# Kernel tuning notes

Hardware: AMD Instinct MI355X
Metric: run time of the kernel (lower is better)

The kernel has to match this reference:

```python
import jax, jax.numpy as jnp
import numpy as np

N, E = 50000, 800000
IN_C, HID, HEADS, LAT = 128, 64, 2, 32
NEG_SLOPE = 0.2  # PyG GATConv default LeakyReLU slope


def gat_layer(x, src, dst, W, att_src, att_dst, bias, heads, out_ch, concat, n):
    # Linear projection, per-head: [n, heads, out_ch]
    h = (x @ W).reshape(n, heads, out_ch)
    a_src = jnp.einsum('nhc,hc->nh', h, att_src)  # [n, heads]
    a_dst = jnp.einsum('nhc,hc->nh', h, att_dst)
    # Per-edge attention logits (edge j->i uses src j, dst i)
    alpha = jax.nn.leaky_relu(a_src[src] + a_dst[dst], negative_slope=NEG_SLOPE)  # [e, heads]
    # Segment softmax over incoming edges of each destination node
    amax = jax.ops.segment_max(alpha, dst, num_segments=n)
    ealpha = jnp.exp(alpha - amax[dst])
    denom = jax.ops.segment_sum(ealpha, dst, num_segments=n)
    alpha = ealpha / (denom[dst] + 1e-16)
    # Weighted scatter-aggregate of source features
    msg = h[src] * alpha[:, :, None]  # [e, heads, out_ch]
    out = jax.ops.segment_sum(msg, dst, num_segments=n)  # [n, heads, out_ch]
    out = out.reshape(n, heads * out_ch) if concat else out.mean(axis=1)
    return out + bias


def setup_inputs() -> dict:
    key = jax.random.key(0)
    ks = jax.random.split(key, 16)
    x = jax.random.normal(ks[0], (N, IN_C), dtype=jnp.float32)
    edge_index = jax.random.randint(ks[1], (2, E), 0, N, dtype=jnp.int32).astype(jnp.int64)
    s = 0.1
    W1 = jax.random.normal(ks[2], (IN_C, HEADS * HID), dtype=jnp.float32) * s
    att_src1 = jax.random.normal(ks[3], (HEADS, HID), dtype=jnp.float32) * s
    att_dst1 = jax.random.normal(ks[4], (HEADS, HID), dtype=jnp.float32) * s
    b1 = jnp.zeros((HEADS * HID,), dtype=jnp.float32)
    Wmu = jax.random.normal(ks[5], (HEADS * HID, LAT), dtype=jnp.float32) * s
    att_src_mu = jax.random.normal(ks[6], (1, LAT), dtype=jnp.float32) * s
    att_dst_mu = jax.random.normal(ks[7], (1, LAT), dtype=jnp.float32) * s
    bmu = jnp.zeros((LAT,), dtype=jnp.float32)
    Wlv = jax.random.normal(ks[8], (HEADS * HID, LAT), dtype=jnp.float32) * s
    att_src_lv = jax.random.normal(ks[9], (1, LAT), dtype=jnp.float32) * s
    att_dst_lv = jax.random.normal(ks[10], (1, LAT), dtype=jnp.float32) * s
    blv = jnp.zeros((LAT,), dtype=jnp.float32)
    return {"x": x, "edge_index": edge_index, "W1": W1, "att_src1": att_src1,
            "att_dst1": att_dst1, "b1": b1, "Wmu": Wmu, "att_src_mu": att_src_mu,
            "att_dst_mu": att_dst_mu, "bmu": bmu, "Wlv": Wlv,
            "att_src_lv": att_src_lv, "att_dst_lv": att_dst_lv, "blv": blv}


def reference(x, edge_index, W1, att_src1, att_dst1, b1,
              Wmu, att_src_mu, att_dst_mu, bmu,
              Wlv, att_src_lv, att_dst_lv, blv):
    n = x.shape[0]
    # PyG GATConv adds self-loops by default
    loops = jnp.arange(n, dtype=edge_index.dtype)
    src = jnp.concatenate([edge_index[0], loops])
    dst = jnp.concatenate([edge_index[1], loops])
    h = gat_layer(x, src, dst, W1, att_src1, att_dst1, b1, HEADS, HID, True, n)
    h = jax.nn.elu(h)
    mu = gat_layer(h, src, dst, Wmu, att_src_mu, att_dst_mu, bmu, 1, LAT, False, n)
    logvar = gat_layer(h, src, dst, Wlv, att_src_lv, att_dst_lv, blv, 1, LAT, False, n)
    return (mu, logvar)
```

## Files before the change

### kernel.cpp

```cpp
#include <hip/hip_runtime.h>
#include <hip/hip_bf16.h>

#define N_NODES 50000
#define N_EDGES 800000
#define EP (N_EDGES + N_NODES)
#define IN_C 128
#define HID 64
#define HEADS 2
#define LAT 32
#define NEG_SLOPE 0.2f
#define MAXDEG 256
#define NBUCKET 391
#define BCAP 3072
#define CHUNK 4096

typedef __attribute__((ext_vector_type(8))) short bf16x8;
typedef __attribute__((ext_vector_type(4))) float f32x4;

__device__ __forceinline__ unsigned short f2bf(float f) {
  unsigned u = __float_as_uint(f);
  u += 0x7FFF + ((u >> 16) & 1);
  return (unsigned short)(u >> 16);
}
__device__ __forceinline__ float bf_lo(unsigned u) { return __uint_as_float(u << 16); }
__device__ __forceinline__ float bf_hi(unsigned u) { return __uint_as_float(u & 0xFFFF0000u); }

__device__ __forceinline__ bf16x8 pack_bf8(const float* __restrict__ p) {
  float4 a = *(const float4*)p;
  float4 b = *(const float4*)(p + 4);
  bf16x8 r;
  r[0] = (short)f2bf(a.x); r[1] = (short)f2bf(a.y);
  r[2] = (short)f2bf(a.z); r[3] = (short)f2bf(a.w);
  r[4] = (short)f2bf(b.x); r[5] = (short)f2bf(b.y);
  r[6] = (short)f2bf(b.z); r[7] = (short)f2bf(b.w);
  return r;
}

__global__ void cursor_init_kernel(int* __restrict__ cursor) {
  int b = threadIdx.x;
  if (b < NBUCKET) cursor[b] = b * BCAP;
}

__global__ __launch_bounds__(256) void bucket_scatter_kernel(
    const int* __restrict__ ei, int* __restrict__ cursor,
    unsigned* __restrict__ csr) {
  __shared__ int histL[512];
  __shared__ int baseL[512];
  __shared__ int gbaseL[512];
  __shared__ int wsumS[4];
  __shared__ int nvalS;
  __shared__ unsigned staging[CHUNK];
  __shared__ unsigned short bktidL[CHUNK];
  const int t = threadIdx.x, lane = t & 63, wid = t >> 6;
  for (int i = t; i < 512; i += 256) histL[i] = 0;
  __syncthreads();
  int myb[CHUNK / 256];
  int myloc[CHUNK / 256];
  unsigned mypay[CHUNK / 256];
  #pragma unroll
  for (int i = 0; i < CHUNK / 256; ++i) {
    int e = blockIdx.x * CHUNK + i * 256 + t;
    if (e < EP) {
      int s, d;
      if (e < N_EDGES) { s = ei[e]; d = ei[N_EDGES + e]; }
      else { s = d = e - N_EDGES; }
      int b = d >> 7;
      myb[i] = b;
      mypay[i] = ((unsigned)(d & 127) << 17) | (unsigned)s;
      myloc[i] = atomicAdd(&histL[b], 1);
    } else myb[i] = -1;
  }
  __syncthreads();
  {
    int v0 = histL[2 * t], v1 = histL[2 * t + 1];
    int pair = v0 + v1, inc = pair;
    #pragma unroll
    for (int off = 1; off < 64; off <<= 1) {
      int nv = __shfl_up(inc, off);
      if (lane >= off) inc += nv;
    }
    if (lane == 63) wsumS[wid] = inc;
    __syncthreads();
    if (t == 0) {
      int run = 0;
      #pragma unroll
      for (int w = 0; w < 4; ++w) { int c = wsumS[w]; wsumS[w] = run; run += c; }
      nvalS = run;
    }
    __syncthreads();
    int excl = wsumS[wid] + inc - pair;
    baseL[2 * t] = excl;
    baseL[2 * t + 1] = excl + v0;
  }
  __syncthreads();
  #pragma unroll
  for (int i = 0; i < CHUNK / 256; ++i)
    if (myb[i] >= 0) {
      int p = baseL[myb[i]] + myloc[i];
      staging[p] = mypay[i];
      bktidL[p] = (unsigned short)myb[i];
    }
  for (int b = t; b < NBUCKET; b += 256) {
    int c = histL[b];
    gbaseL[b] = c ? atomicAdd(&cursor[b], c) : 0;
  }
  __syncthreads();
  const int nval = nvalS;
  for (int j = t; j < nval; j += 256) {
    int b = bktidL[j];
    int pos = gbaseL[b] + (j - baseL[b]);
    if (pos < (b + 1) * BCAP) csr[pos] = staging[j];
  }
}

__global__ __launch_bounds__(256) void bucket_fill_kernel(
    const int* __restrict__ cursor, unsigned* __restrict__ csr,
    int* __restrict__ counts, int* __restrict__ cend) {
  __shared__ unsigned eseg[BCAP];
  __shared__ int hist[128];
  __shared__ int basef[128];
  __shared__ int cur[128];
  const int b = blockIdx.x, t = threadIdx.x;
  const int segbase = b * BCAP;
  int cnt = cursor[b] - segbase;
  if (cnt > BCAP) cnt = BCAP;
  if (t < 128) hist[t] = 0;
  __syncthreads();
  for (int j = t; j < cnt; j += 256) {
    unsigned u = csr[segbase + j];
    eseg[j] = u;
    atomicAdd(&hist[u >> 17], 1);
  }
  __syncthreads();
  if (t < 64) {
    int v0 = hist[2 * t], v1 = hist[2 * t + 1];
    int pair = v0 + v1, inc = pair;
    #pragma unroll
    for (int off = 1; off < 64; off <<= 1) {
      int nv = __shfl_up(inc, off);
      if (t >= off) inc += nv;
    }
    int excl = inc - pair;
    basef[2 * t] = excl;
    basef[2 * t + 1] = excl + v0;
  }
  __syncthreads();
  if (t < 128) {
    cur[t] = basef[t];
    int n = b * 128 + t;
    if (n < N_NODES) {
      counts[n] = hist[t];
      cend[n] = segbase + basef[t] + hist[t];
    }
  }
  __syncthreads();
  for (int j = t; j < cnt; j += 256) {
    unsigned u = eseg[j];
    int dl = u >> 17;
    int p = atomicAdd(&cur[dl], 1);
    csr[segbase + p] = u & 0x1FFFF;
  }
}

__global__ __launch_bounds__(256) void proj1_kernel(
    const float* __restrict__ x, const float* __restrict__ W,
    unsigned short* __restrict__ h1b) {
  __shared__ unsigned short Wb[16384];
  const int t = threadIdx.x;
  for (int i = t; i < 128 * 128; i += 256) {
    int k = i >> 7, n = i & 127;
    int kk = k >> 5, q = (k >> 3) & 3, j = k & 7;
    Wb[((((kk << 2) + q) << 7) + n) * 8 + j] = f2bf(W[i]);
  }
  __syncthreads();
  const int w = t >> 6, lane = t & 63;
  const int m = lane & 15, quad = lane >> 4;
  const int row0 = blockIdx.x * 32;
  const int n0 = w * 32;
  f32x4 acc[2][2] = {};
  #pragma unroll
  for (int kk = 0; kk < 4; ++kk) {
    bf16x8 afr[2], bfr[2];
    #pragma unroll
    for (int mt = 0; mt < 2; ++mt) {
      int row = row0 + mt * 16 + m;
      if (row >= N_NODES) row = N_NODES - 1;
      afr[mt] = pack_bf8(x + (size_t)row * 128 + kk * 32 + quad * 8);
    }
    #pragma unroll
    for (int nt = 0; nt < 2; ++nt)
      bfr[nt] = *(const bf16x8*)&Wb[((((kk << 2) + quad) << 7) + n0 + nt * 16 + m) * 8];
    #pragma unroll
    for (int mt = 0; mt < 2; ++mt)
      #pragma unroll
      for (int nt = 0; nt < 2; ++nt)
        acc[mt][nt] = __builtin_amdgcn_mfma_f32_16x16x32_bf16(
            afr[mt], bfr[nt], acc[mt][nt], 0, 0, 0);
  }
  #pragma unroll
  for (int mt = 0; mt < 2; ++mt)
    #pragma unroll
    for (int r = 0; r < 4; ++r) {
      int row = row0 + mt * 16 + quad * 4 + r;
      if (row < N_NODES) {
        #pragma unroll
        for (int nt = 0; nt < 2; ++nt)
          h1b[(size_t)row * 128 + n0 + nt * 16 + m] = f2bf(acc[mt][nt][r]);
      }
    }
}

__global__ __launch_bounds__(256) void a1_kernel(
    const unsigned* __restrict__ h1b2, const float* __restrict__ att_src,
    const float* __restrict__ att_dst, float* __restrict__ a1) {
  const int n = blockIdx.x * 4 + (threadIdx.x >> 6);
  const int lane = threadIdx.x & 63;
  unsigned u = h1b2[(size_t)n * 64 + lane];
  float h0 = bf_lo(u), h1v = bf_hi(u);
  int head = lane >> 5;
  int cc = (lane * 2) & 63;
  float s = h0 * att_src[head * HID + cc] + h1v * att_src[head * HID + cc + 1];
  float d = h0 * att_dst[head * HID + cc] + h1v * att_dst[head * HID + cc + 1];
  #pragma unroll
  for (int off = 16; off; off >>= 1) {
    s += __shfl_xor(s, off);
    d += __shfl_xor(d, off);
  }
  if ((lane & 31) == 0) {
    a1[n * 4 + head] = s;
    a1[n * 4 + 2 + head] = d;
  }
}

__global__ __launch_bounds__(64) void agg1_csr_kernel(
    const int* __restrict__ counts, const int* __restrict__ cend,
    const unsigned* __restrict__ csr_src, const float4* __restrict__ a1,
    const unsigned* __restrict__ h1b2, const float* __restrict__ b,
    float* __restrict__ hact) {
  __shared__ float w_lds[2][MAXDEG];
  __shared__ int   s_lds[MAXDEG];
  const int n = blockIdx.x;
  const int t = threadIdx.x;
  const int end = cend[n];
  int cnt = counts[n];
  if (cnt > MAXDEG) cnt = MAXDEG;
  const int beg = end - cnt;
  const float4 bv = a1[n];
  float p0 = 0.f, p1 = 0.f;
  for (int i = t; i < cnt; i += 64) {
    int s = (int)csr_src[beg + i];
    float4 av = a1[s];
    float l0 = av.x + bv.z; l0 = l0 > 0.f ? l0 : NEG_SLOPE * l0;
    float l1 = av.y + bv.w; l1 = l1 > 0.f ? l1 : NEG_SLOPE * l1;
    float e0 = expf(l0), e1 = expf(l1);
    w_lds[0][i] = e0; w_lds[1][i] = e1; s_lds[i] = s;
    p0 += e0; p1 += e1;
  }
  #pragma unroll
  for (int off = 32; off; off >>= 1) {
    p0 += __shfl_xor(p0, off);
    p1 += __shfl_xor(p1, off);
  }
  __syncthreads();
  const int head = t >> 5;
  const unsigned* hp = h1b2 + t;
  float ax = 0.f, ay = 0.f;
  #pragma unroll 4
  for (int i = 0; i < cnt; ++i) {
    int s = s_lds[i];
    float w = w_lds[head][i];
    unsigned u = hp[(size_t)s * 64];
    ax += bf_lo(u) * w; ay += bf_hi(u) * w;
  }
  float inv = 1.f / ((head ? p1 : p0) + 1e-16f);
  float vx = ax * inv + b[t * 2];
  float vy = ay * inv + b[t * 2 + 1];
  vx = vx > 0.f ? vx : (expf(vx) - 1.f);
  vy = vy > 0.f ? vy : (expf(vy) - 1.f);
  *(float2*)(hact + (size_t)n * 128 + t * 2) = make_float2(vx, vy);
}

__global__ __launch_bounds__(256) void proj2_kernel(
    const float* __restrict__ h, const float* __restrict__ Wmu,
    const float* __restrict__ Wlv, unsigned short* __restrict__ h2b) {
  __shared__ unsigned short Wb[8192];
  const int t = threadIdx.x;
  for (int i = t; i < 128 * 64; i += 256) {
    int k = i >> 6, n = i & 63;
    float v = (n < 32) ? Wmu[k * 32 + n] : Wlv[k * 32 + (n - 32)];
    int kk = k >> 5, q = (k >> 3) & 3, j = k & 7;
    Wb[((((kk << 2) + q) << 6) + n) * 8 + j] = f2bf(v);
  }
  __syncthreads();
  const int w = t >> 6, lane = t & 63;
  const int m = lane & 15, quad = lane >> 4;
  const int row0 = blockIdx.x * 64 + (w >> 1) * 32;
  const int n0 = (w & 1) * 32;
  f32x4 acc[2][2] = {};
  #pragma unroll
  for (int kk = 0; kk < 4; ++kk) {
    bf16x8 afr[2], bfr[2];
    #pragma unroll
    for (int mt = 0; mt < 2; ++mt) {
      int row = row0 + mt * 16 + m;
      if (row >= N_NODES) row = N_NODES - 1;
      afr[mt] = pack_bf8(h + (size_t)row * 128 + kk * 32 + quad * 8);
    }
    #pragma unroll
    for (int nt = 0; nt < 2; ++nt)
      bfr[nt] = *(const bf16x8*)&Wb[((((kk << 2) + quad) << 6) + n0 + nt * 16 + m) * 8];
    #pragma unroll
    for (int mt = 0; mt < 2; ++mt)
      #pragma unroll
      for (int nt = 0; nt < 2; ++nt)
        acc[mt][nt] = __builtin_amdgcn_mfma_f32_16x16x32_bf16(
            afr[mt], bfr[nt], acc[mt][nt], 0, 0, 0);
  }
  #pragma unroll
  for (int mt = 0; mt < 2; ++mt)
    #pragma unroll
    for (int r = 0; r < 4; ++r) {
      int row = row0 + mt * 16 + quad * 4 + r;
      if (row < N_NODES) {
        #pragma unroll
        for (int nt = 0; nt < 2; ++nt)
          h2b[(size_t)row * 64 + n0 + nt * 16 + m] = f2bf(acc[mt][nt][r]);
      }
    }
}

__global__ __launch_bounds__(256) void a2_kernel(
    const unsigned short* __restrict__ h2b, const float* __restrict__ asmu,
    const float* __restrict__ admu, const float* __restrict__ aslv,
    const float* __restrict__ adlv, float* __restrict__ a2) {
  const int n = blockIdx.x * 4 + (threadIdx.x >> 6);
  const int lane = threadIdx.x & 63;
  float h = __uint_as_float(((unsigned)h2b[(size_t)n * 64 + lane]) << 16);
  int j = lane >> 5, o = lane & 31;
  float s = h * (j ? aslv : asmu)[o];
  float d = h * (j ? adlv : admu)[o];
  #pragma unroll
  for (int off = 16; off; off >>= 1) {
    s += __shfl_xor(s, off);
    d += __shfl_xor(d, off);
  }
  if (o == 0) {
    a2[n * 4 + j * 2 + 0] = s;
    a2[n * 4 + j * 2 + 1] = d;
  }
}

__global__ __launch_bounds__(64) void agg2_csr_kernel(
    const int* __restrict__ counts, const int* __restrict__ cend,
    const unsigned* __restrict__ csr_src, const float4* __restrict__ a2,
    const unsigned short* __restrict__ h2b,
    const float* __restrict__ bmu, const float* __restrict__ blv,
    float* __restrict__ out) {
  __shared__ float w_lds[2][MAXDEG];
  __shared__ int   s_lds[MAXDEG];
  const int n = blockIdx.x;
  const int t = threadIdx.x;
  const int end = cend[n];
  int cnt = counts[n];
  if (cnt > MAXDEG) cnt = MAXDEG;
  const int beg = end - cnt;
  const float4 bv = a2[n];
  float p0 = 0.f, p1 = 0.f;
  for (int i = t; i < cnt; i += 64) {
    int s = (int)csr_src[beg + i];
    float4 av = a2[s];
    float l0 = av.x + bv.y; l0 = l0 > 0.f ? l0 : NEG_SLOPE * l0;
    float l1 = av.z + bv.w; l1 = l1 > 0.f ? l1 : NEG_SLOPE * l1;
    float e0 = expf(l0), e1 = expf(l1);
    w_lds[0][i] = e0; w_lds[1][i] = e1; s_lds[i] = s;
    p0 += e0; p1 += e1;
  }
  #pragma unroll
  for (int off = 32; off; off >>= 1) {
    p0 += __shfl_xor(p0, off);
    p1 += __shfl_xor(p1, off);
  }
  __syncthreads();
  const int j = t >> 5, o = t & 31;
  const unsigned short* hp = h2b + t;
  float acc = 0.f;
  #pragma unroll 4
  for (int i = 0; i < cnt; ++i) {
    int s = s_lds[i];
    float hv = __uint_as_float(((unsigned)hp[(size_t)s * 64]) << 16);
    acc += hv * w_lds[j][i];
  }
  float inv = 1.f / ((j ? p1 : p0) + 1e-16f);
  out[(size_t)j * N_NODES * LAT + (size_t)n * LAT + o] =
      acc * inv + (j ? blv : bmu)[o];
}

extern "C" void kernel_launch(void* const* d_in, const int* in_sizes, int n_in,
                              void* d_out, int out_size, void* d_ws, size_t ws_size,
                              hipStream_t stream) {
  const float* x        = (const float*)d_in[0];
  const int* ei         = (const int*)d_in[1];
  const float* W1       = (const float*)d_in[2];
  const float* att_src1 = (const float*)d_in[3];
  const float* att_dst1 = (const float*)d_in[4];
  const float* b1       = (const float*)d_in[5];
  const float* Wmu      = (const float*)d_in[6];
  const float* asmu     = (const float*)d_in[7];
  const float* admu     = (const float*)d_in[8];
  const float* bmu      = (const float*)d_in[9];
  const float* Wlv      = (const float*)d_in[10];
  const float* aslv     = (const float*)d_in[11];
  const float* adlv     = (const float*)d_in[12];
  const float* blv      = (const float*)d_in[13];
  float* out = (float*)d_out;

  float* ws   = (float*)d_ws;
  float* hact = ws;
  float* a1   = hact + (size_t)N_NODES * 128;
  float* a2   = a1 + (size_t)N_NODES * 4;
  unsigned short* h1b = (unsigned short*)(a2 + (size_t)N_NODES * 4);
  unsigned short* h2b = h1b + (size_t)N_NODES * 128;
  int* counts = (int*)(h2b + (size_t)N_NODES * 64);
  int* cend   = counts + N_NODES;
  int* cursor = cend + N_NODES;
  unsigned* csr = (unsigned*)(cursor + NBUCKET);

  cursor_init_kernel<<<1, 512, 0, stream>>>(cursor);
  bucket_scatter_kernel<<<(EP + CHUNK - 1) / CHUNK, 256, 0, stream>>>(ei, cursor, csr);
  bucket_fill_kernel<<<NBUCKET, 256, 0, stream>>>(cursor, csr, counts, cend);

  proj1_kernel<<<(N_NODES + 31) / 32, 256, 0, stream>>>(x, W1, h1b);
  a1_kernel<<<N_NODES / 4, 256, 0, stream>>>(
      (const unsigned*)h1b, att_src1, att_dst1, a1);
  agg1_csr_kernel<<<N_NODES, 64, 0, stream>>>(
      counts, cend, csr, (const float4*)a1, (const unsigned*)h1b, b1, hact);

  proj2_kernel<<<(N_NODES + 63) / 64, 256, 0, stream>>>(hact, Wmu, Wlv, h2b);
  a2_kernel<<<N_NODES / 4, 256, 0, stream>>>(h2b, asmu, admu, aslv, adlv, a2);
  agg2_csr_kernel<<<N_NODES, 64, 0, stream>>>(
      counts, cend, csr, (const float4*)a2, h2b, bmu, blv, out);
}
```

Before: 238.2 us.

## Fuse edge bucketing with layer-1 projection and fold attention logits into projections

Merges the edge bucket-scatter and layer-1 projection into one launch that splits blocks by index, sharing LDS through a union. The attention dot products (a1, a2) are now computed from the MFMA accumulators inside the projection kernels, so the separate a1/a2 kernels that re-read h1b/h2b are removed. Cursor init becomes a memset with relative offsets. This cuts four launches and two passes over the projected features, at the cost of LDS atomics and fp32-vs-bf16 logits that differ slightly from before.

After: 220.2 us. 1.08x faster.

```diff
diff --git a/kernel.cpp b/kernel.cpp
--- a/kernel.cpp
+++ b/kernel.cpp
@@ -13,6 +13,8 @@
 #define NBUCKET 391
 #define BCAP 3072
 #define CHUNK 4096
+#define NSCAT ((EP + CHUNK - 1) / CHUNK)
+#define NPROJ1 ((N_NODES + 31) / 32)
 
 typedef __attribute__((ext_vector_type(8))) short bf16x8;
 typedef __attribute__((ext_vector_type(4))) float f32x4;
@@ -36,80 +38,160 @@
   return r;
 }
 
-__global__ void cursor_init_kernel(int* __restrict__ cursor) {
-  int b = threadIdx.x;
-  if (b < NBUCKET) cursor[b] = b * BCAP;
-}
-
-__global__ __launch_bounds__(256) void bucket_scatter_kernel(
+struct ScatSmem {
+  int histL[512];
+  int baseL[512];
+  int gbaseL[512];
+  int wsumS[4];
+  int nvalS;
+  unsigned staging[CHUNK];
+  unsigned short bktidL[CHUNK];
+};
+struct Proj1Smem {
+  unsigned short Wb[16384];
+  float part[32][4];
+};
+union K1Smem { ScatSmem sc; Proj1Smem pj; };
+
+__global__ __launch_bounds__(256) void k1_kernel(
     const int* __restrict__ ei, int* __restrict__ cursor,
-    unsigned* __restrict__ csr) {
-  __shared__ int histL[512];
-  __shared__ int baseL[512];
-  __shared__ int gbaseL[512];
-  __shared__ int wsumS[4];
-  __shared__ int nvalS;
-  __shared__ unsigned staging[CHUNK];
-  __shared__ unsigned short bktidL[CHUNK];
+    unsigned* __restrict__ csr,
+    const float* __restrict__ x, const float* __restrict__ W,
+    const float* __restrict__ att_src, const float* __restrict__ att_dst,
+    unsigned short* __restrict__ h1b, float* __restrict__ a1) {
+  __shared__ K1Smem sm;
   const int t = threadIdx.x, lane = t & 63, wid = t >> 6;
-  for (int i = t; i < 512; i += 256) histL[i] = 0;
-  __syncthreads();
-  int myb[CHUNK / 256];
-  int myloc[CHUNK / 256];
-  unsigned mypay[CHUNK / 256];
-  #pragma unroll
-  for (int i = 0; i < CHUNK / 256; ++i) {
-    int e = blockIdx.x * CHUNK + i * 256 + t;
-    if (e < EP) {
-      int s, d;
-      if (e < N_EDGES) { s = ei[e]; d = ei[N_EDGES + e]; }
-      else { s = d = e - N_EDGES; }
-      int b = d >> 7;
-      myb[i] = b;
-      mypay[i] = ((unsigned)(d & 127) << 17) | (unsigned)s;
-      myloc[i] = atomicAdd(&histL[b], 1);
-    } else myb[i] = -1;
-  }
-  __syncthreads();
-  {
-    int v0 = histL[2 * t], v1 = histL[2 * t + 1];
-    int pair = v0 + v1, inc = pair;
-    #pragma unroll
-    for (int off = 1; off < 64; off <<= 1) {
-      int nv = __shfl_up(inc, off);
-      if (lane >= off) inc += nv;
-    }
-    if (lane == 63) wsumS[wid] = inc;
-    __syncthreads();
-    if (t == 0) {
-      int run = 0;
-      #pragma unroll
-      for (int w = 0; w < 4; ++w) { int c = wsumS[w]; wsumS[w] = run; run += c; }
-      nvalS = run;
-    }
-    __syncthreads();
-    int excl = wsumS[wid] + inc - pair;
-    baseL[2 * t] = excl;
-    baseL[2 * t + 1] = excl + v0;
-  }
-  __syncthreads();
-  #pragma unroll
-  for (int i = 0; i < CHUNK / 256; ++i)
-    if (myb[i] >= 0) {
-      int p = baseL[myb[i]] + myloc[i];
-      staging[p] = mypay[i];
-      bktidL[p] = (unsigned short)myb[i];
-    }
-  for (int b = t; b < NBUCKET; b += 256) {
-    int c = histL[b];
-    gbaseL[b] = c ? atomicAdd(&cursor[b], c) : 0;
-  }
-  __syncthreads();
-  const int nval = nvalS;
-  for (int j = t; j < nval; j += 256) {
-    int b = bktidL[j];
-    int pos = gbaseL[b] + (j - baseL[b]);
-    if (pos < (b + 1) * BCAP) csr[pos] = staging[j];
+
+  if (blockIdx.x < NSCAT) {
+    for (int i = t; i < 512; i += 256) sm.sc.histL[i] = 0;
+    __syncthreads();
+    int myb[CHUNK / 256];
+    int myloc[CHUNK / 256];
+    unsigned mypay[CHUNK / 256];
+    #pragma unroll
+    for (int i = 0; i < CHUNK / 256; ++i) {
+      int e = blockIdx.x * CHUNK + i * 256 + t;
+      if (e < EP) {
+        int s, d;
+        if (e < N_EDGES) { s = ei[e]; d = ei[N_EDGES + e]; }
+        else { s = d = e - N_EDGES; }
+        int b = d >> 7;
+        myb[i] = b;
+        mypay[i] = ((unsigned)(d & 127) << 17) | (unsigned)s;
+        myloc[i] = atomicAdd(&sm.sc.histL[b], 1);
+      } else myb[i] = -1;
+    }
+    __syncthreads();
+    {
+      int v0 = sm.sc.histL[2 * t], v1 = sm.sc.histL[2 * t + 1];
+      int pair = v0 + v1, inc = pair;
+      #pragma unroll
+      for (int off = 1; off < 64; off <<= 1) {
+        int nv = __shfl_up(inc, off);
+        if (lane >= off) inc += nv;
+      }
+      if (lane == 63) sm.sc.wsumS[wid] = inc;
+      __syncthreads();
+      if (t == 0) {
+        int run = 0;
+        #pragma unroll
+        for (int w = 0; w < 4; ++w) { int c = sm.sc.wsumS[w]; sm.sc.wsumS[w] = run; run += c; }
+        sm.sc.nvalS = run;
+      }
+      __syncthreads();
+      int excl = sm.sc.wsumS[wid] + inc - pair;
+      sm.sc.baseL[2 * t] = excl;
+      sm.sc.baseL[2 * t + 1] = excl + v0;
+    }
+    __syncthreads();
+    #pragma unroll
+    for (int i = 0; i < CHUNK / 256; ++i)
+      if (myb[i] >= 0) {
+        int p = sm.sc.baseL[myb[i]] + myloc[i];
+        sm.sc.staging[p] = mypay[i];
+        sm.sc.bktidL[p] = (unsigned short)myb[i];
+      }
+    for (int b = t; b < NBUCKET; b += 256) {
+      int c = sm.sc.histL[b];
+      sm.sc.gbaseL[b] = c ? atomicAdd(&cursor[b], c) : 0;
+    }
+    __syncthreads();
+    const int nval = sm.sc.nvalS;
+    for (int j = t; j < nval; j += 256) {
+      int b = sm.sc.bktidL[j];
+      int off = sm.sc.gbaseL[b] + (j - sm.sc.baseL[b]);
+      if (off < BCAP) csr[b * BCAP + off] = sm.sc.staging[j];
+    }
+  } else {
+    const int pb = blockIdx.x - NSCAT;
+    for (int i = t; i < 128 * 128; i += 256) {
+      int k = i >> 7, n = i & 127;
+      int kk = k >> 5, q = (k >> 3) & 3, j = k & 7;
+      sm.pj.Wb[((((kk << 2) + q) << 7) + n) * 8 + j] = f2bf(W[i]);
+    }
+    if (t < 128) ((float*)sm.pj.part)[t] = 0.f;
+    __syncthreads();
+    const int w = wid;
+    const int m = lane & 15, quad = lane >> 4;
+    const int row0 = pb * 32;
+    const int n0 = w * 32;
+    const int head = w >> 1;
+    f32x4 acc[2][2] = {};
+    #pragma unroll
+    for (int kk = 0; kk < 4; ++kk) {
+      bf16x8 afr[2], bfr[2];
+      #pragma unroll
+      for (int mt = 0; mt < 2; ++mt) {
+        int row = row0 + mt * 16 + m;
+        if (row >= N_NODES) row = N_NODES - 1;
+        afr[mt] = pack_bf8(x + (size_t)row * 128 + kk * 32 + quad * 8);
+      }
+      #pragma unroll
+      for (int nt = 0; nt < 2; ++nt)
+        bfr[nt] = *(const bf16x8*)&sm.pj.Wb[((((kk << 2) + quad) << 7) + n0 + nt * 16 + m) * 8];
+      #pragma unroll
+      for (int mt = 0; mt < 2; ++mt)
+        #pragma unroll
+        for (int nt = 0; nt < 2; ++nt)
+          acc[mt][nt] = __builtin_amdgcn_mfma_f32_16x16x32_bf16(
+              afr[mt], bfr[nt], acc[mt][nt], 0, 0, 0);
+    }
+    float asv[2], adv[2];
+    #pragma unroll
+    for (int nt = 0; nt < 2; ++nt) {
+      int cc = ((n0 & 63) + nt * 16 + m);
+      asv[nt] = att_src[head * HID + cc];
+      adv[nt] = att_dst[head * HID + cc];
+    }
+    #pragma unroll
+    for (int mt = 0; mt < 2; ++mt)
+      #pragma unroll
+      for (int r = 0; r < 4; ++r) {
+        int row = row0 + mt * 16 + quad * 4 + r;
+        if (row < N_NODES) {
+          #pragma unroll
+          for (int nt = 0; nt < 2; ++nt)
+            h1b[(size_t)row * 128 + n0 + nt * 16 + m] = f2bf(acc[mt][nt][r]);
+        }
+        float s = acc[mt][0][r] * asv[0] + acc[mt][1][r] * asv[1];
+        float d = acc[mt][0][r] * adv[0] + acc[mt][1][r] * adv[1];
+        #pragma unroll
+        for (int off = 8; off; off >>= 1) {
+          s += __shfl_xor(s, off);
+          d += __shfl_xor(d, off);
+        }
+        if (m == 0) {
+          atomicAdd(&sm.pj.part[mt * 16 + quad * 4 + r][head], s);
+          atomicAdd(&sm.pj.part[mt * 16 + quad * 4 + r][2 + head], d);
+        }
+      }
+    __syncthreads();
+    if (t < 32) {
+      int row = row0 + t;
+      if (row < N_NODES)
+        *(float4*)&a1[(size_t)row * 4] = make_float4(
+            sm.pj.part[t][0], sm.pj.part[t][1], sm.pj.part[t][2], sm.pj.part[t][3]);
+    }
   }
 }
 
@@ -122,7 +204,7 @@
   __shared__ int cur[128];
   const int b = blockIdx.x, t = threadIdx.x;
   const int segbase = b * BCAP;
-  int cnt = cursor[b] - segbase;
+  int cnt = cursor[b];
   if (cnt > BCAP) cnt = BCAP;
   if (t < 128) hist[t] = 0;
   __syncthreads();
@@ -159,76 +241,6 @@
     int dl = u >> 17;
     int p = atomicAdd(&cur[dl], 1);
     csr[segbase + p] = u & 0x1FFFF;
-  }
-}
-
-__global__ __launch_bounds__(256) void proj1_kernel(
-    const float* __restrict__ x, const float* __restrict__ W,
-    unsigned short* __restrict__ h1b) {
-  __shared__ unsigned short Wb[16384];
-  const int t = threadIdx.x;
-  for (int i = t; i < 128 * 128; i += 256) {
-    int k = i >> 7, n = i & 127;
-    int kk = k >> 5, q = (k >> 3) & 3, j = k & 7;
-    Wb[((((kk << 2) + q) << 7) + n) * 8 + j] = f2bf(W[i]);
-  }
-  __syncthreads();
-  const int w = t >> 6, lane = t & 63;
-  const int m = lane & 15, quad = lane >> 4;
-  const int row0 = blockIdx.x * 32;
-  const int n0 = w * 32;
-  f32x4 acc[2][2] = {};
-  #pragma unroll
-  for (int kk = 0; kk < 4; ++kk) {
-    bf16x8 afr[2], bfr[2];
-    #pragma unroll
-    for (int mt = 0; mt < 2; ++mt) {
-      int row = row0 + mt * 16 + m;
-      if (row >= N_NODES) row = N_NODES - 1;
-      afr[mt] = pack_bf8(x + (size_t)row * 128 + kk * 32 + quad * 8);
-    }
-    #pragma unroll
-    for (int nt = 0; nt < 2; ++nt)
-      bfr[nt] = *(const bf16x8*)&Wb[((((kk << 2) + quad) << 7) + n0 + nt * 16 + m) * 8];
-    #pragma unroll
-    for (int mt = 0; mt < 2; ++mt)
-      #pragma unroll
-      for (int nt = 0; nt < 2; ++nt)
-        acc[mt][nt] = __builtin_amdgcn_mfma_f32_16x16x32_bf16(
-            afr[mt], bfr[nt], acc[mt][nt], 0, 0, 0);
-  }
-  #pragma unroll
-  for (int mt = 0; mt < 2; ++mt)
-    #pragma unroll
-    for (int r = 0; r < 4; ++r) {
-      int row = row0 + mt * 16 + quad * 4 + r;
-      if (row < N_NODES) {
-        #pragma unroll
-        for (int nt = 0; nt < 2; ++nt)
-          h1b[(size_t)row * 128 + n0 + nt * 16 + m] = f2bf(acc[mt][nt][r]);
-      }
-    }
-}
-
-__global__ __launch_bounds__(256) void a1_kernel(
-    const unsigned* __restrict__ h1b2, const float* __restrict__ att_src,
-    const float* __restrict__ att_dst, float* __restrict__ a1) {
-  const int n = blockIdx.x * 4 + (threadIdx.x >> 6);
-  const int lane = threadIdx.x & 63;
-  unsigned u = h1b2[(size_t)n * 64 + lane];
-  float h0 = bf_lo(u), h1v = bf_hi(u);
-  int head = lane >> 5;
-  int cc = (lane * 2) & 63;
-  float s = h0 * att_src[head * HID + cc] + h1v * att_src[head * HID + cc + 1];
-  float d = h0 * att_dst[head * HID + cc] + h1v * att_dst[head * HID + cc + 1];
-  #pragma unroll
-  for (int off = 16; off; off >>= 1) {
-    s += __shfl_xor(s, off);
-    d += __shfl_xor(d, off);
-  }
-  if ((lane & 31) == 0) {
-    a1[n * 4 + head] = s;
-    a1[n * 4 + 2 + head] = d;
   }
 }
 
@@ -282,7 +294,10 @@
 
 __global__ __launch_bounds__(256) void proj2_kernel(
     const float* __restrict__ h, const float* __restrict__ Wmu,
-    const float* __restrict__ Wlv, unsigned short* __restrict__ h2b) {
+    const float* __restrict__ Wlv,
+    const float* __restrict__ asmu, const float* __restrict__ admu,
+    const float* __restrict__ aslv, const float* __restrict__ adlv,
+    unsigned short* __restrict__ h2b, float* __restrict__ a2) {
   __shared__ unsigned short Wb[8192];
   const int t = threadIdx.x;
   for (int i = t; i < 128 * 64; i += 256) {
@@ -295,7 +310,8 @@
   const int w = t >> 6, lane = t & 63;
   const int m = lane & 15, quad = lane >> 4;
   const int row0 = blockIdx.x * 64 + (w >> 1) * 32;
-  const int n0 = (w & 1) * 32;
+  const int j = w & 1;
+  const int n0 = j * 32;
   f32x4 acc[2][2] = {};
   #pragma unroll
   for (int kk = 0; kk < 4; ++kk) {
@@ -315,6 +331,13 @@
       for (int nt = 0; nt < 2; ++nt)
         acc[mt][nt] = __builtin_amdgcn_mfma_f32_16x16x32_bf16(
             afr[mt], bfr[nt], acc[mt][nt], 0, 0, 0);
+  }
+  float asv[2], adv[2];
+  #pragma unroll
+  for (int nt = 0; nt < 2; ++nt) {
+    int o = nt * 16 + m;
+    asv[nt] = (j ? aslv : asmu)[o];
+    adv[nt] = (j ? adlv : admu)[o];
   }
   #pragma unroll
   for (int mt = 0; mt < 2; ++mt)
@@ -326,28 +349,18 @@
         for (int nt = 0; nt < 2; ++nt)
           h2b[(size_t)row * 64 + n0 + nt * 16 + m] = f2bf(acc[mt][nt][r]);
       }
-    }
-}
-
-__global__ __launch_bounds__(256) void a2_kernel(
-    const unsigned short* __restrict__ h2b, const float* __restrict__ asmu,
-    const float* __restrict__ admu, const float* __restrict__ aslv,
-    const float* __restrict__ adlv, float* __restrict__ a2) {
-  const int n = blockIdx.x * 4 + (threadIdx.x >> 6);
-  const int lane = threadIdx.x & 63;
-  float h = __uint_as_float(((unsigned)h2b[(size_t)n * 64 + lane]) << 16);
-  int j = lane >> 5, o = lane & 31;
-  float s = h * (j ? aslv : asmu)[o];
-  float d = h * (j ? adlv : admu)[o];
-  #pragma unroll
-  for (int off = 16; off; off >>= 1) {
-    s += __shfl_xor(s, off);
-    d += __shfl_xor(d, off);
-  }
-  if (o == 0) {
-    a2[n * 4 + j * 2 + 0] = s;
-    a2[n * 4 + j * 2 + 1] = d;
-  }
+      float s = acc[mt][0][r] * asv[0] + acc[mt][1][r] * asv[1];
+      float d = acc[mt][0][r] * adv[0] + acc[mt][1][r] * adv[1];
+      #pragma unroll
+      for (int off = 8; off; off >>= 1) {
+        s += __shfl_xor(s, off);
+        d += __shfl_xor(d, off);
+      }
+      if (m == 0 && row < N_NODES) {
+        a2[(size_t)row * 4 + j * 2 + 0] = s;
+        a2[(size_t)row * 4 + j * 2 + 1] = d;
+      }
+    }
 }
 
 __global__ __launch_bounds__(64) void agg2_csr_kernel(
@@ -425,18 +438,15 @@
   int* cursor = cend + N_NODES;
   unsigned* csr = (unsigned*)(cursor + NBUCKET);
 
-  cursor_init_kernel<<<1, 512, 0, stream>>>(cursor);
-  bucket_scatter_kernel<<<(EP + CHUNK - 1) / CHUNK, 256, 0, stream>>>(ei, cursor, csr);
+  hipMemsetAsync(cursor, 0, NBUCKET * sizeof(int), stream);
+
+  k1_kernel<<<NSCAT + NPROJ1, 256, 0, stream>>>(
+      ei, cursor, csr, x, W1, att_src1, att_dst1, h1b, a1);
   bucket_fill_kernel<<<NBUCKET, 256, 0, stream>>>(cursor, csr, counts, cend);
-
-  proj1_kernel<<<(N_NODES + 31) / 32, 256, 0, stream>>>(x, W1, h1b);
-  a1_kernel<<<N_NODES / 4, 256, 0, stream>>>(
-      (const unsigned*)h1b, att_src1, att_dst1, a1);
   agg1_csr_kernel<<<N_NODES, 64, 0, stream>>>(
       counts, cend, csr, (const float4*)a1, (const unsigned*)h1b, b1, hact);
-
-  proj2_kernel<<<(N_NODES + 63) / 64, 256, 0, stream>>>(hact, Wmu, Wlv, h2b);
-  a2_kernel<<<N_NODES / 4, 256, 0, stream>>>(h2b, asmu, admu, aslv, adlv, a2);
+  proj2_kernel<<<(N_NODES + 63) / 64, 256, 0, stream>>>(
+      hact, Wmu, Wlv, asmu, admu, aslv, adlv, h2b, a2);
   agg2_csr_kernel<<<N_NODES, 64, 0, stream>>>(
       counts, cend, csr, (const float4*)a2, h2b, bmu, blv, out);
 }
```
